# Kernel optimization log

Hardware: AMD Instinct MI355X
Metric: run time of the kernel (lower is better)

## Reference

```python
import jax, jax.numpy as jnp
import numpy as np
import math

JOINT_NAMES = ['pelvis', 'hip_R', 'hip_L', 'knee_R', 'knee_L', 'ankle_R', 'ankle_L', 'trunk', 'shoulder_R', 'shoulder_L', 'elbow_R', 'elbow_L']
KINEMATIC_CHAINS = {'pelvis': ['hip_R', 'hip_L', 'trunk'], 'hip_R': ['pelvis', 'knee_R'], 'hip_L': ['pelvis', 'knee_L'], 'knee_R': ['hip_R', 'ankle_R'], 'knee_L': ['hip_L', 'ankle_L'], 'ankle_R': ['knee_R'], 'ankle_L': ['knee_L'], 'trunk': ['pelvis', 'shoulder_R', 'shoulder_L'], 'shoulder_R': ['trunk', 'elbow_R'], 'shoulder_L': ['trunk', 'elbow_L'], 'elbow_R': ['shoulder_R'], 'elbow_L': ['shoulder_L']}

D_MODEL = 128
N_HEADS = 4
HEAD_DIM = D_MODEL // N_HEADS
B = 16384
N = 12

def build_adjacency_matrix():
    n = len(JOINT_NAMES)
    adj = np.zeros((n, n), dtype=np.float32)
    idx = {name: i for i, name in enumerate(JOINT_NAMES)}
    for joint, neighbors in KINEMATIC_CHAINS.items():
        i = idx[joint]
        for nb in neighbors:
            j = idx[nb]
            adj[i, j] = 1.0
            adj[j, i] = 1.0
    adj = adj + np.eye(n, dtype=np.float32)
    return jnp.asarray(adj)

def setup_inputs() -> dict:
    key = jax.random.key(0)
    ks = jax.random.split(key, 12)
    s = 1.0 / math.sqrt(D_MODEL)  # torch Linear default init scale
    inp = {
        'x': jax.random.normal(ks[0], (B, N, D_MODEL), dtype=jnp.float32),
        'visibility': jax.random.uniform(ks[1], (B, N), dtype=jnp.float32),
        'Wq': jax.random.uniform(ks[2], (D_MODEL, D_MODEL), jnp.float32, -s, s),
        'bq': jax.random.uniform(ks[3], (D_MODEL,), jnp.float32, -s, s),
        'Wk': jax.random.uniform(ks[4], (D_MODEL, D_MODEL), jnp.float32, -s, s),
        'bk': jax.random.uniform(ks[5], (D_MODEL,), jnp.float32, -s, s),
        'Wv': jax.random.uniform(ks[6], (D_MODEL, D_MODEL), jnp.float32, -s, s),
        'bv': jax.random.uniform(ks[7], (D_MODEL,), jnp.float32, -s, s),
        'Wo': jax.random.uniform(ks[8], (D_MODEL, D_MODEL), jnp.float32, -s, s),
        'bo': jax.random.uniform(ks[9], (D_MODEL,), jnp.float32, -s, s),
        'bias_scale': jnp.asarray(1.0, dtype=jnp.float32),
        'adjacency': build_adjacency_matrix(),
    }
    return inp

def reference(x, visibility, Wq, bq, Wk, bk, Wv, bv, Wo, bo, bias_scale, adjacency):
    Bsz, Nj, D = x.shape
    # projections; weights stored as (out,in) like torch Linear -> x @ W.T + b
    def proj(W, b):
        return (jnp.einsum('bnd,ed->bne', x, W) + b).reshape(Bsz, Nj, N_HEADS, HEAD_DIM).transpose(0, 2, 1, 3)
    q = proj(Wq, bq)  # (B, H, N, hd)
    k = proj(Wk, bk)
    v = proj(Wv, bv)
    scores = jnp.einsum('bhnd,bhmd->bhnm', q, k) / math.sqrt(HEAD_DIM)
    scores = scores + adjacency[None, None, :, :] * bias_scale
    # visibility mask: subtract 10 where key joint is not visible
    scores = scores - 10.0 * (1.0 - visibility[:, None, None, :])
    attn = jax.nn.softmax(scores, axis=-1)
    out = jnp.einsum('bhnm,bhmd->bhnd', attn, v)
    out = out.transpose(0, 2, 1, 3).reshape(Bsz, Nj, D)
    out = jnp.einsum('bnd,ed->bne', out, Wo) + bo
    return out
```

## Files before the change

kernel.cpp:

```cpp
#include <hip/hip_runtime.h>


typedef unsigned short u16;
typedef short bf16x8 __attribute__((ext_vector_type(8)));
typedef short bf16x4 __attribute__((ext_vector_type(4)));
typedef float f32x4 __attribute__((ext_vector_type(4)));

#define MFMA(a, b, c) __builtin_amdgcn_mfma_f32_16x16x32_bf16((a), (b), (c), 0, 0, 0)

#define BPW   4
#define ROWS  (BPW * 12)
#define XPAD  136
#define VPAD  20
#define PPAD  20

struct SMem {
    u16   qs[ROWS * XPAD];
    u16   ks[ROWS * XPAD];
    u16   vT[BPW * 128 * VPAD];
    u16   P[4 * 16 * PPAD];
    float bias_s[16 * 16];
    float vis_s[BPW * 16];
    float bvec[4 * 128];
    float rls[4 * 16];
};

__device__ __forceinline__ u16 f2b(float f) {
    unsigned u = __builtin_bit_cast(unsigned, f);
    return (u16)((u + 0x7fffu + ((u >> 16) & 1u)) >> 16);
}

__device__ __forceinline__ void st4(u16* p, float a, float b, float c, float d) {
    ushort4 v; v.x = f2b(a); v.y = f2b(b); v.z = f2b(c); v.w = f2b(d);
    *(ushort4*)p = v;
}

__device__ __forceinline__ bf16x8 pack8(float4 a, float4 b) {
    bf16x8 r;
    r[0] = (short)f2b(a.x); r[1] = (short)f2b(a.y);
    r[2] = (short)f2b(a.z); r[3] = (short)f2b(a.w);
    r[4] = (short)f2b(b.x); r[5] = (short)f2b(b.y);
    r[6] = (short)f2b(b.z); r[7] = (short)f2b(b.w);
    return r;
}

__global__ void prep_w(const float* __restrict__ Wq, const float* __restrict__ Wk,
                       const float* __restrict__ Wv, const float* __restrict__ Wo,
                       u16* __restrict__ wbf) {
    int i = blockIdx.x * 256 + threadIdx.x;
    wbf[i]         = f2b(Wq[i]);
    wbf[16384 + i] = f2b(Wk[i]);
    wbf[32768 + i] = f2b(Wv[i]);
    wbf[49152 + i] = f2b(Wo[i]);
}

__global__ __launch_bounds__(256, 3) void cja_main(
    const float* __restrict__ x, const float* __restrict__ vis,
    const float* __restrict__ bq, const float* __restrict__ bk,
    const float* __restrict__ bv, const float* __restrict__ bo,
    const float* __restrict__ bias_scale, const float* __restrict__ adj,
    const u16* __restrict__ wbf, float* __restrict__ out)
{
    extern __shared__ char smraw[];
    SMem& sm = *(SMem*)smraw;

    const int tid  = threadIdx.x;
    const int wave = tid >> 6;
    const int lane = tid & 63;
    const int lq   = lane >> 4;
    const int lm   = lane & 15;
    const int b0   = blockIdx.x * BPW;

    for (int i = tid; i < BPW * 128; i += 256) {
        unsigned* d = (unsigned*)(sm.vT + i * VPAD + 12);
        d[0] = 0u; d[1] = 0u; d[2] = 0u; d[3] = 0u;
    }
    {
        const float L2E = 1.4426950408889634f;
        float scale = bias_scale[0] * L2E;
        int n = tid >> 4, m = tid & 15;
        float bval;
        if (m >= 12)     bval = -1e30f;
        else if (n < 12) bval = adj[n * 12 + m] * scale;
        else             bval = 0.0f;
        sm.bias_s[tid] = bval;
        if (tid < BPW * 16) {
            int bb = tid >> 4, mm = tid & 15;
            sm.vis_s[tid] = (mm < 12) ? 10.0f * L2E * (1.0f - vis[(size_t)(b0 + bb) * 12 + mm])
                                      : 0.0f;
        }
        if (tid < 128) {
            sm.bvec[tid]       = bq[tid];
            sm.bvec[128 + tid] = bk[tid];
            sm.bvec[256 + tid] = bv[tid];
            sm.bvec[384 + tid] = bo[tid];
        }
    }
    __syncthreads();

    {
        const u16* Wq_b = wbf;
        const u16* Wk_b = wbf + 16384;
        const u16* Wv_b = wbf + 32768;
        const float* xw = x + (size_t)b0 * 1536;
        f32x4 accq[2][3], acck[2][3], accv[3][2];
        #pragma unroll
        for (int i = 0; i < 2; i++)
            #pragma unroll
            for (int j = 0; j < 3; j++) { accq[i][j] = (f32x4){0,0,0,0}; acck[i][j] = (f32x4){0,0,0,0}; }
        #pragma unroll
        for (int i = 0; i < 3; i++)
            #pragma unroll
            for (int j = 0; j < 2; j++) accv[i][j] = (f32x4){0,0,0,0};

        const int mrow0 = wave * 32 + lm;
        const int mrow1 = mrow0 + 16;
        #pragma unroll
        for (int ks2 = 0; ks2 < 4; ks2++) {
            const int koff = ks2 * 32 + lq * 8;
            bf16x8 xf[3];
            #pragma unroll
            for (int nt = 0; nt < 3; nt++) {
                const float* xp = xw + (nt * 16 + lm) * 128 + koff;
                float4 u0 = *(const float4*)xp;
                float4 u1 = *(const float4*)(xp + 4);
                xf[nt] = pack8(u0, u1);
            }
            bf16x8 wq0 = *(const bf16x8*)(Wq_b + mrow0 * 128 + koff);
            bf16x8 wq1 = *(const bf16x8*)(Wq_b + mrow1 * 128 + koff);
            bf16x8 wk0 = *(const bf16x8*)(Wk_b + mrow0 * 128 + koff);
            bf16x8 wk1 = *(const bf16x8*)(Wk_b + mrow1 * 128 + koff);
            bf16x8 wv0 = *(const bf16x8*)(Wv_b + mrow0 * 128 + koff);
            bf16x8 wv1 = *(const bf16x8*)(Wv_b + mrow1 * 128 + koff);
            #pragma unroll
            for (int nt = 0; nt < 3; nt++) {
                accq[0][nt] = MFMA(wq0, xf[nt], accq[0][nt]);
                accq[1][nt] = MFMA(wq1, xf[nt], accq[1][nt]);
                acck[0][nt] = MFMA(wk0, xf[nt], acck[0][nt]);
                acck[1][nt] = MFMA(wk1, xf[nt], acck[1][nt]);
                accv[nt][0] = MFMA(xf[nt], wv0, accv[nt][0]);
                accv[nt][1] = MFMA(xf[nt], wv1, accv[nt][1]);
            }
        }
        #pragma unroll
        for (int mi = 0; mi < 2; mi++) {
            const int e0 = (wave * 2 + mi) * 16 + lq * 4;
            float bq0 = sm.bvec[e0], bq1 = sm.bvec[e0+1], bq2 = sm.bvec[e0+2], bq3 = sm.bvec[e0+3];
            float bk0 = sm.bvec[128+e0], bk1 = sm.bvec[128+e0+1], bk2 = sm.bvec[128+e0+2], bk3 = sm.bvec[128+e0+3];
            #pragma unroll
            for (int nt = 0; nt < 3; nt++) {
                const int n = nt * 16 + lm;
                st4(sm.qs + n * XPAD + e0, accq[mi][nt][0]+bq0, accq[mi][nt][1]+bq1,
                                           accq[mi][nt][2]+bq2, accq[mi][nt][3]+bq3);
                st4(sm.ks + n * XPAD + e0, acck[mi][nt][0]+bk0, acck[mi][nt][1]+bk1,
                                           acck[mi][nt][2]+bk2, acck[mi][nt][3]+bk3);
            }
        }
        #pragma unroll
        for (int nt2 = 0; nt2 < 2; nt2++) {
            const int e = (wave * 2 + nt2) * 16 + lm;
            const float bvv = sm.bvec[256 + e];
            #pragma unroll
            for (int mt = 0; mt < 3; mt++) {
                #pragma unroll
                for (int r = 0; r < 4; r++) {
                    int n = mt * 16 + lq * 4 + r;
                    int bb = n / 12, j = n - bb * 12;
                    sm.vT[bb * (128 * VPAD) + e * VPAD + j] = f2b(accv[mt][nt2][r] + bvv);
                }
            }
        }
    }
    __syncthreads();

    {
        const int bl   = wave;
        const int nql  = (lm < 12) ? lm : 11;
        const u16* qrowp = sm.qs + (bl * 12 + nql) * XPAD;
        const u16* krowp = sm.ks + (bl * 12 + nql) * XPAD;
        const float vism = sm.vis_s[bl * 16 + lm];
        float bias_b[4];
        #pragma unroll
        for (int r = 0; r < 4; r++) bias_b[r] = sm.bias_s[(lq * 4 + r) * 16 + lm];
        u16*   Pw  = sm.P + wave * (16 * PPAD);
        float* rlw = sm.rls + wave * 16;
        const u16* vTb = sm.vT + bl * (128 * VPAD);
        const float SC2 = 0.2550348606381560f;
        const bf16x8 z8 = {0,0,0,0,0,0,0,0};
        #pragma unroll
        for (int h = 0; h < 4; h++) {
            bf16x8 qa = *(const bf16x8*)(qrowp + h * 32 + lq * 8);
            bf16x8 kb = *(const bf16x8*)(krowp + h * 32 + lq * 8);
            f32x4 sc = MFMA(qa, kb, ((f32x4){0,0,0,0}));
            #pragma unroll
            for (int r = 0; r < 4; r++) {
                float s2 = sc[r] * SC2 + bias_b[r] - vism;
                float e  = __builtin_amdgcn_exp2f(s2);
                float l  = e;
                l += __shfl_xor(l, 1, 16);
                l += __shfl_xor(l, 2, 16);
                l += __shfl_xor(l, 4, 16);
                l += __shfl_xor(l, 8, 16);
                Pw[(lq * 4 + r) * PPAD + lm] = f2b(e);
                if (lm == 0) rlw[lq * 4 + r] = __builtin_amdgcn_rcpf(l);
            }
            float rln = rlw[lm];
            bf16x8 pb = z8;
            if (lq < 2) {
                const bf16x4* pp = (const bf16x4*)(Pw + lm * PPAD + lq * 8);
                pb = __builtin_shufflevector(pp[0], pp[1], 0, 1, 2, 3, 4, 5, 6, 7);
            }
            #pragma unroll
            for (int mt = 0; mt < 2; mt++) {
                bf16x8 va = z8;
                if (lq < 2) {
                    const bf16x4* vp = (const bf16x4*)(vTb + (h * 32 + mt * 16 + lm) * VPAD + lq * 8);
                    va = __builtin_shufflevector(vp[0], vp[1], 0, 1, 2, 3, 4, 5, 6, 7);
                }
                f32x4 c = MFMA(va, pb, ((f32x4){0,0,0,0}));
                if (lm < 12) {
                    u16* d = sm.qs + (bl * 12 + lm) * XPAD + h * 32 + mt * 16 + lq * 4;
                    st4(d, c[0] * rln, c[1] * rln, c[2] * rln, c[3] * rln);
                }
            }
        }
    }
    __syncthreads();

    {
        const u16* Wo_b = wbf + 49152;
        f32x4 acc[2][3];
        #pragma unroll
        for (int i = 0; i < 2; i++)
            #pragma unroll
            for (int j = 0; j < 3; j++) acc[i][j] = (f32x4){0,0,0,0};
        const int m0 = wave * 32 + lm;
        #pragma unroll
        for (int ks2 = 0; ks2 < 4; ks2++) {
            const int koff = ks2 * 32 + lq * 8;
            bf16x8 a0 = *(const bf16x8*)(Wo_b + m0 * 128 + koff);
            bf16x8 a1 = *(const bf16x8*)(Wo_b + (m0 + 16) * 128 + koff);
            #pragma unroll
            for (int nt = 0; nt < 3; nt++) {
                bf16x8 bfr = *(const bf16x8*)(sm.qs + (nt * 16 + lm) * XPAD + koff);
                acc[0][nt] = MFMA(a0, bfr, acc[0][nt]);
                acc[1][nt] = MFMA(a1, bfr, acc[1][nt]);
            }
        }
        #pragma unroll
        for (int mi = 0; mi < 2; mi++) {
            const int e0 = (wave * 2 + mi) * 16 + lq * 4;
            float bo0 = sm.bvec[384+e0], bo1 = sm.bvec[384+e0+1],
                  bo2 = sm.bvec[384+e0+2], bo3 = sm.bvec[384+e0+3];
            #pragma unroll
            for (int nt = 0; nt < 3; nt++) {
                const int n = nt * 16 + lm;
                float4 o;
                o.x = acc[mi][nt][0] + bo0;
                o.y = acc[mi][nt][1] + bo1;
                o.z = acc[mi][nt][2] + bo2;
                o.w = acc[mi][nt][3] + bo3;
                *(float4*)(out + ((size_t)(b0 * 12 + n) << 7) + e0) = o;
            }
        }
    }
}

extern "C" void kernel_launch(void* const* d_in, const int* in_sizes, int n_in,
                              void* d_out, int out_size, void* d_ws, size_t ws_size,
                              hipStream_t stream) {
    const float* x   = (const float*)d_in[0];
    const float* vis = (const float*)d_in[1];
    const float* Wq  = (const float*)d_in[2];
    const float* bq  = (const float*)d_in[3];
    const float* Wk  = (const float*)d_in[4];
    const float* bk  = (const float*)d_in[5];
    const float* Wv  = (const float*)d_in[6];
    const float* bv  = (const float*)d_in[7];
    const float* Wo  = (const float*)d_in[8];
    const float* bo  = (const float*)d_in[9];
    const float* bs  = (const float*)d_in[10];
    const float* adj = (const float*)d_in[11];
    u16* wbf = (u16*)d_ws;

    prep_w<<<64, 256, 0, stream>>>(Wq, Wk, Wv, Wo, wbf);
    cja_main<<<16384 / BPW, 256, sizeof(SMem), stream>>>(
        x, vis, bq, bk, bv, bo, bs, adj, wbf, (float*)d_out);
}
```

Baseline: 288.2 us.

## Make blocks persistent over four batch groups and prefetch next x during attention

```diff
diff --git a/kernel.cpp b/kernel.cpp
--- a/kernel.cpp
+++ b/kernel.cpp
@@ -13,6 +13,7 @@
 #define XPAD  136
 #define VPAD  20
 #define PPAD  20
+#define GPW   4
 
 struct SMem {
     u16   qs[ROWS * XPAD];
@@ -69,14 +70,35 @@
     const int lane = tid & 63;
     const int lq   = lane >> 4;
     const int lm   = lane & 15;
-    const int b0   = blockIdx.x * BPW;
+    const int grp0 = blockIdx.x * GPW;
+
+    float4 xr[12][2];
+    bf16x8 xf[12];
+
+    auto issue_x = [&](int grp) {
+        const float* xw = x + (size_t)grp * (BPW * 12 * 128);
+        #pragma unroll
+        for (int ks2 = 0; ks2 < 4; ks2++)
+            #pragma unroll
+            for (int nt = 0; nt < 3; nt++) {
+                const float* xp = xw + (nt * 16 + lm) * 128 + ks2 * 32 + lq * 8;
+                xr[ks2 * 3 + nt][0] = *(const float4*)xp;
+                xr[ks2 * 3 + nt][1] = *(const float4*)(xp + 4);
+            }
+    };
+    auto pack_x = [&]() {
+        #pragma unroll
+        for (int i = 0; i < 12; i++) xf[i] = pack8(xr[i][0], xr[i][1]);
+    };
+
+    issue_x(grp0);
 
     for (int i = tid; i < BPW * 128; i += 256) {
         unsigned* d = (unsigned*)(sm.vT + i * VPAD + 12);
         d[0] = 0u; d[1] = 0u; d[2] = 0u; d[3] = 0u;
     }
+    const float L2E = 1.4426950408889634f;
     {
-        const float L2E = 1.4426950408889634f;
         float scale = bias_scale[0] * L2E;
         int n = tid >> 4, m = tid & 15;
         float bval;
@@ -84,11 +106,6 @@
         else if (n < 12) bval = adj[n * 12 + m] * scale;
         else             bval = 0.0f;
         sm.bias_s[tid] = bval;
-        if (tid < BPW * 16) {
-            int bb = tid >> 4, mm = tid & 15;
-            sm.vis_s[tid] = (mm < 12) ? 10.0f * L2E * (1.0f - vis[(size_t)(b0 + bb) * 12 + mm])
-                                      : 0.0f;
-        }
         if (tid < 128) {
             sm.bvec[tid]       = bq[tid];
             sm.bvec[128 + tid] = bk[tid];
@@ -96,171 +113,212 @@
             sm.bvec[384 + tid] = bo[tid];
         }
     }
+    pack_x();
     __syncthreads();
 
+    const int bl  = wave;
+    const int nql = (lm < 12) ? lm : 11;
+    const u16* qrowp = sm.qs + (bl * 12 + nql) * XPAD;
+    const u16* krowp = sm.ks + (bl * 12 + nql) * XPAD;
+    u16*   Pw  = sm.P + wave * (16 * PPAD);
+    float* rlw = sm.rls + wave * 16;
+    const u16* vTb = sm.vT + bl * (128 * VPAD);
+    const int mrow0 = wave * 32 + lm;
+    const int mrow1 = mrow0 + 16;
+    float bias_b[4];
+    #pragma unroll
+    for (int rr = 0; rr < 4; rr++) bias_b[rr] = sm.bias_s[(lq * 4 + rr) * 16 + lm];
+
+    f32x4 oacc[2][3];
+
+    #pragma unroll 1
+    for (int rnd = 0; rnd < GPW; ++rnd) {
+        const int grp = grp0 + rnd;
+        const int b0  = grp * BPW;
+
+        if (rnd > 0) {
+            const int b0p = b0 - BPW;
+            #pragma unroll
+            for (int mi = 0; mi < 2; mi++) {
+                const int e0 = (wave * 2 + mi) * 16 + lq * 4;
+                #pragma unroll
+                for (int nt = 0; nt < 3; nt++) {
+                    const int n = nt * 16 + lm;
+                    *(f32x4*)(out + ((size_t)(b0p * 12 + n) << 7) + e0) = oacc[mi][nt];
+                }
+            }
+        }
+
+        if (tid < 64) {
+            int bb = tid >> 4, mm = tid & 15;
+            sm.vis_s[tid] = (mm < 12) ? 10.0f * L2E * (1.0f - vis[(size_t)(b0 + bb) * 12 + mm])
+                                      : 0.0f;
+        }
+
+        {
+            const u16* Wq_b = wbf;
+            const u16* Wk_b = wbf + 16384;
+            f32x4 accq[2][3], acck[2][3];
+            #pragma unroll
+            for (int i = 0; i < 2; i++)
+                #pragma unroll
+                for (int j = 0; j < 3; j++) { accq[i][j] = (f32x4){0,0,0,0}; acck[i][j] = (f32x4){0,0,0,0}; }
+            #pragma unroll
+            for (int ks2 = 0; ks2 < 4; ks2++) {
+                const int koff = ks2 * 32 + lq * 8;
+                bf16x8 wq0 = *(const bf16x8*)(Wq_b + mrow0 * 128 + koff);
+                bf16x8 wq1 = *(const bf16x8*)(Wq_b + mrow1 * 128 + koff);
+                bf16x8 wk0 = *(const bf16x8*)(Wk_b + mrow0 * 128 + koff);
+                bf16x8 wk1 = *(const bf16x8*)(Wk_b + mrow1 * 128 + koff);
+                #pragma unroll
+                for (int nt = 0; nt < 3; nt++) {
+                    accq[0][nt] = MFMA(wq0, xf[ks2*3+nt], accq[0][nt]);
+                    accq[1][nt] = MFMA(wq1, xf[ks2*3+nt], accq[1][nt]);
+                    acck[0][nt] = MFMA(wk0, xf[ks2*3+nt], acck[0][nt]);
+                    acck[1][nt] = MFMA(wk1, xf[ks2*3+nt], acck[1][nt]);
+                }
+            }
+            #pragma unroll
+            for (int mi = 0; mi < 2; mi++) {
+                const int e0 = (wave * 2 + mi) * 16 + lq * 4;
+                float bq0 = sm.bvec[e0], bq1 = sm.bvec[e0+1], bq2 = sm.bvec[e0+2], bq3 = sm.bvec[e0+3];
+                float bk0 = sm.bvec[128+e0], bk1 = sm.bvec[128+e0+1], bk2 = sm.bvec[128+e0+2], bk3 = sm.bvec[128+e0+3];
+                #pragma unroll
+                for (int nt = 0; nt < 3; nt++) {
+                    const int n = nt * 16 + lm;
+                    st4(sm.qs + n * XPAD + e0, accq[mi][nt][0]+bq0, accq[mi][nt][1]+bq1,
+                                               accq[mi][nt][2]+bq2, accq[mi][nt][3]+bq3);
+                    st4(sm.ks + n * XPAD + e0, acck[mi][nt][0]+bk0, acck[mi][nt][1]+bk1,
+                                               acck[mi][nt][2]+bk2, acck[mi][nt][3]+bk3);
+                }
+            }
+            const u16* Wv_b = wbf + 32768;
+            f32x4 accv[3][2];
+            #pragma unroll
+            for (int i = 0; i < 3; i++)
+                #pragma unroll
+                for (int j = 0; j < 2; j++) accv[i][j] = (f32x4){0,0,0,0};
+            #pragma unroll
+            for (int ks2 = 0; ks2 < 4; ks2++) {
+                const int koff = ks2 * 32 + lq * 8;
+                bf16x8 wv0 = *(const bf16x8*)(Wv_b + mrow0 * 128 + koff);
+                bf16x8 wv1 = *(const bf16x8*)(Wv_b + mrow1 * 128 + koff);
+                #pragma unroll
+                for (int nt = 0; nt < 3; nt++) {
+                    accv[nt][0] = MFMA(xf[ks2*3+nt], wv0, accv[nt][0]);
+                    accv[nt][1] = MFMA(xf[ks2*3+nt], wv1, accv[nt][1]);
+                }
+            }
+            #pragma unroll
+            for (int nt2 = 0; nt2 < 2; nt2++) {
+                const int e = (wave * 2 + nt2) * 16 + lm;
+                const float bvv = sm.bvec[256 + e];
+                #pragma unroll
+                for (int mt = 0; mt < 3; mt++) {
+                    #pragma unroll
+                    for (int r = 0; r < 4; r++) {
+                        int n = mt * 16 + lq * 4 + r;
+                        int bb = n / 12, j = n - bb * 12;
+                        sm.vT[bb * (128 * VPAD) + e * VPAD + j] = f2b(accv[mt][nt2][r] + bvv);
+                    }
+                }
+            }
+        }
+        __syncthreads();
+
+        {
+            if (rnd + 1 < GPW) issue_x(grp + 1);
+
+            const float vism = sm.vis_s[bl * 16 + lm];
+            const float SC2 = 0.2550348606381560f;
+            const bf16x8 z8 = {0,0,0,0,0,0,0,0};
+            #pragma unroll
+            for (int h = 0; h < 4; h++) {
+                bf16x8 qa = *(const bf16x8*)(qrowp + h * 32 + lq * 8);
+                bf16x8 kb = *(const bf16x8*)(krowp + h * 32 + lq * 8);
+                f32x4 sc = MFMA(qa, kb, ((f32x4){0,0,0,0}));
+                #pragma unroll
+                for (int r = 0; r < 4; r++) {
+                    float s2 = sc[r] * SC2 + bias_b[r] - vism;
+                    float e  = __builtin_amdgcn_exp2f(s2);
+                    float l  = e;
+                    l += __shfl_xor(l, 1, 16);
+                    l += __shfl_xor(l, 2, 16);
+                    l += __shfl_xor(l, 4, 16);
+                    l += __shfl_xor(l, 8, 16);
+                    Pw[(lq * 4 + r) * PPAD + lm] = f2b(e);
+                    if (lm == 0) rlw[lq * 4 + r] = __builtin_amdgcn_rcpf(l);
+                }
+                float rln = rlw[lm];
+                bf16x8 pb = z8;
+                if (lq < 2) {
+                    const bf16x4* pp = (const bf16x4*)(Pw + lm * PPAD + lq * 8);
+                    pb = __builtin_shufflevector(pp[0], pp[1], 0, 1, 2, 3, 4, 5, 6, 7);
+                }
+                #pragma unroll
+                for (int mt = 0; mt < 2; mt++) {
+                    bf16x8 va = z8;
+                    if (lq < 2) {
+                        const bf16x4* vp = (const bf16x4*)(vTb + (h * 32 + mt * 16 + lm) * VPAD + lq * 8);
+                        va = __builtin_shufflevector(vp[0], vp[1], 0, 1, 2, 3, 4, 5, 6, 7);
+                    }
+                    f32x4 c = MFMA(va, pb, ((f32x4){0,0,0,0}));
+                    if (lm < 12) {
+                        u16* d = sm.qs + (bl * 12 + lm) * XPAD + h * 32 + mt * 16 + lq * 4;
+                        st4(d, c[0] * rln, c[1] * rln, c[2] * rln, c[3] * rln);
+                    }
+                }
+            }
+
+            if (rnd + 1 < GPW) pack_x();
+        }
+        __syncthreads();
+
+        {
+            const u16* Wo_b = wbf + 49152;
+            f32x4 acc[2][3];
+            #pragma unroll
+            for (int i = 0; i < 2; i++)
+                #pragma unroll
+                for (int j = 0; j < 3; j++) acc[i][j] = (f32x4){0,0,0,0};
+            #pragma unroll
+            for (int ks2 = 0; ks2 < 4; ks2++) {
+                const int koff = ks2 * 32 + lq * 8;
+                bf16x8 a0 = *(const bf16x8*)(Wo_b + mrow0 * 128 + koff);
+                bf16x8 a1 = *(const bf16x8*)(Wo_b + (mrow1) * 128 + koff);
+                #pragma unroll
+                for (int nt = 0; nt < 3; nt++) {
+                    bf16x8 bfr = *(const bf16x8*)(sm.qs + (nt * 16 + lm) * XPAD + koff);
+                    acc[0][nt] = MFMA(a0, bfr, acc[0][nt]);
+                    acc[1][nt] = MFMA(a1, bfr, acc[1][nt]);
+                }
+            }
+            #pragma unroll
+            for (int mi = 0; mi < 2; mi++) {
+                const int e0 = (wave * 2 + mi) * 16 + lq * 4;
+                float bo0 = sm.bvec[384+e0], bo1 = sm.bvec[384+e0+1],
+                      bo2 = sm.bvec[384+e0+2], bo3 = sm.bvec[384+e0+3];
+                #pragma unroll
+                for (int nt = 0; nt < 3; nt++) {
+                    oacc[mi][nt][0] = acc[mi][nt][0] + bo0;
+                    oacc[mi][nt][1] = acc[mi][nt][1] + bo1;
+                    oacc[mi][nt][2] = acc[mi][nt][2] + bo2;
+                    oacc[mi][nt][3] = acc[mi][nt][3] + bo3;
+                }
+            }
+        }
+        if (rnd + 1 < GPW) __syncthreads();
+    }
+
     {
-        const u16* Wq_b = wbf;
-        const u16* Wk_b = wbf + 16384;
-        const u16* Wv_b = wbf + 32768;
-        const float* xw = x + (size_t)b0 * 1536;
-        f32x4 accq[2][3], acck[2][3], accv[3][2];
-        #pragma unroll
-        for (int i = 0; i < 2; i++)
-            #pragma unroll
-            for (int j = 0; j < 3; j++) { accq[i][j] = (f32x4){0,0,0,0}; acck[i][j] = (f32x4){0,0,0,0}; }
-        #pragma unroll
-        for (int i = 0; i < 3; i++)
-            #pragma unroll
-            for (int j = 0; j < 2; j++) accv[i][j] = (f32x4){0,0,0,0};
-
-        const int mrow0 = wave * 32 + lm;
-        const int mrow1 = mrow0 + 16;
-        #pragma unroll
-        for (int ks2 = 0; ks2 < 4; ks2++) {
-            const int koff = ks2 * 32 + lq * 8;
-            bf16x8 xf[3];
-            #pragma unroll
-            for (int nt = 0; nt < 3; nt++) {
-                const float* xp = xw + (nt * 16 + lm) * 128 + koff;
-                float4 u0 = *(const float4*)xp;
-                float4 u1 = *(const float4*)(xp + 4);
-                xf[nt] = pack8(u0, u1);
-            }
-            bf16x8 wq0 = *(const bf16x8*)(Wq_b + mrow0 * 128 + koff);
-            bf16x8 wq1 = *(const bf16x8*)(Wq_b + mrow1 * 128 + koff);
-            bf16x8 wk0 = *(const bf16x8*)(Wk_b + mrow0 * 128 + koff);
-            bf16x8 wk1 = *(const bf16x8*)(Wk_b + mrow1 * 128 + koff);
-            bf16x8 wv0 = *(const bf16x8*)(Wv_b + mrow0 * 128 + koff);
-            bf16x8 wv1 = *(const bf16x8*)(Wv_b + mrow1 * 128 + koff);
-            #pragma unroll
-            for (int nt = 0; nt < 3; nt++) {
-                accq[0][nt] = MFMA(wq0, xf[nt], accq[0][nt]);
-                accq[1][nt] = MFMA(wq1, xf[nt], accq[1][nt]);
-                acck[0][nt] = MFMA(wk0, xf[nt], acck[0][nt]);
-                acck[1][nt] = MFMA(wk1, xf[nt], acck[1][nt]);
-                accv[nt][0] = MFMA(xf[nt], wv0, accv[nt][0]);
-                accv[nt][1] = MFMA(xf[nt], wv1, accv[nt][1]);
-            }
-        }
+        const int b0p = (grp0 + GPW - 1) * BPW;
         #pragma unroll
         for (int mi = 0; mi < 2; mi++) {
             const int e0 = (wave * 2 + mi) * 16 + lq * 4;
-            float bq0 = sm.bvec[e0], bq1 = sm.bvec[e0+1], bq2 = sm.bvec[e0+2], bq3 = sm.bvec[e0+3];
-            float bk0 = sm.bvec[128+e0], bk1 = sm.bvec[128+e0+1], bk2 = sm.bvec[128+e0+2], bk3 = sm.bvec[128+e0+3];
             #pragma unroll
             for (int nt = 0; nt < 3; nt++) {
                 const int n = nt * 16 + lm;
-                st4(sm.qs + n * XPAD + e0, accq[mi][nt][0]+bq0, accq[mi][nt][1]+bq1,
-                                           accq[mi][nt][2]+bq2, accq[mi][nt][3]+bq3);
-                st4(sm.ks + n * XPAD + e0, acck[mi][nt][0]+bk0, acck[mi][nt][1]+bk1,
-                                           acck[mi][nt][2]+bk2, acck[mi][nt][3]+bk3);
-            }
-        }
-        #pragma unroll
-        for (int nt2 = 0; nt2 < 2; nt2++) {
-            const int e = (wave * 2 + nt2) * 16 + lm;
-            const float bvv = sm.bvec[256 + e];
-            #pragma unroll
-            for (int mt = 0; mt < 3; mt++) {
-                #pragma unroll
-                for (int r = 0; r < 4; r++) {
-                    int n = mt * 16 + lq * 4 + r;
-                    int bb = n / 12, j = n - bb * 12;
-                    sm.vT[bb * (128 * VPAD) + e * VPAD + j] = f2b(accv[mt][nt2][r] + bvv);
-                }
-            }
-        }
-    }
-    __syncthreads();
-
-    {
-        const int bl   = wave;
-        const int nql  = (lm < 12) ? lm : 11;
-        const u16* qrowp = sm.qs + (bl * 12 + nql) * XPAD;
-        const u16* krowp = sm.ks + (bl * 12 + nql) * XPAD;
-        const float vism = sm.vis_s[bl * 16 + lm];
-        float bias_b[4];
-        #pragma unroll
-        for (int r = 0; r < 4; r++) bias_b[r] = sm.bias_s[(lq * 4 + r) * 16 + lm];
-        u16*   Pw  = sm.P + wave * (16 * PPAD);
-        float* rlw = sm.rls + wave * 16;
-        const u16* vTb = sm.vT + bl * (128 * VPAD);
-        const float SC2 = 0.2550348606381560f;
-        const bf16x8 z8 = {0,0,0,0,0,0,0,0};
-        #pragma unroll
-        for (int h = 0; h < 4; h++) {
-            bf16x8 qa = *(const bf16x8*)(qrowp + h * 32 + lq * 8);
-            bf16x8 kb = *(const bf16x8*)(krowp + h * 32 + lq * 8);
-            f32x4 sc = MFMA(qa, kb, ((f32x4){0,0,0,0}));
-            #pragma unroll
-            for (int r = 0; r < 4; r++) {
-                float s2 = sc[r] * SC2 + bias_b[r] - vism;
-                float e  = __builtin_amdgcn_exp2f(s2);
-                float l  = e;
-                l += __shfl_xor(l, 1, 16);
-                l += __shfl_xor(l, 2, 16);
-                l += __shfl_xor(l, 4, 16);
-                l += __shfl_xor(l, 8, 16);
-                Pw[(lq * 4 + r) * PPAD + lm] = f2b(e);
-                if (lm == 0) rlw[lq * 4 + r] = __builtin_amdgcn_rcpf(l);
-            }
-            float rln = rlw[lm];
-            bf16x8 pb = z8;
-            if (lq < 2) {
-                const bf16x4* pp = (const bf16x4*)(Pw + lm * PPAD + lq * 8);
-                pb = __builtin_shufflevector(pp[0], pp[1], 0, 1, 2, 3, 4, 5, 6, 7);
-            }
-            #pragma unroll
-            for (int mt = 0; mt < 2; mt++) {
-                bf16x8 va = z8;
-                if (lq < 2) {
-                    const bf16x4* vp = (const bf16x4*)(vTb + (h * 32 + mt * 16 + lm) * VPAD + lq * 8);
-                    va = __builtin_shufflevector(vp[0], vp[1], 0, 1, 2, 3, 4, 5, 6, 7);
-                }
-                f32x4 c = MFMA(va, pb, ((f32x4){0,0,0,0}));
-                if (lm < 12) {
-                    u16* d = sm.qs + (bl * 12 + lm) * XPAD + h * 32 + mt * 16 + lq * 4;
-                    st4(d, c[0] * rln, c[1] * rln, c[2] * rln, c[3] * rln);
-                }
-            }
-        }
-    }
-    __syncthreads();
-
-    {
-        const u16* Wo_b = wbf + 49152;
-        f32x4 acc[2][3];
-        #pragma unroll
-        for (int i = 0; i < 2; i++)
-            #pragma unroll
-            for (int j = 0; j < 3; j++) acc[i][j] = (f32x4){0,0,0,0};
-        const int m0 = wave * 32 + lm;
-        #pragma unroll
-        for (int ks2 = 0; ks2 < 4; ks2++) {
-            const int koff = ks2 * 32 + lq * 8;
-            bf16x8 a0 = *(const bf16x8*)(Wo_b + m0 * 128 + koff);
-            bf16x8 a1 = *(const bf16x8*)(Wo_b + (m0 + 16) * 128 + koff);
-            #pragma unroll
-            for (int nt = 0; nt < 3; nt++) {
-                bf16x8 bfr = *(const bf16x8*)(sm.qs + (nt * 16 + lm) * XPAD + koff);
-                acc[0][nt] = MFMA(a0, bfr, acc[0][nt]);
-                acc[1][nt] = MFMA(a1, bfr, acc[1][nt]);
-            }
-        }
-        #pragma unroll
-        for (int mi = 0; mi < 2; mi++) {
-            const int e0 = (wave * 2 + mi) * 16 + lq * 4;
-            float bo0 = sm.bvec[384+e0], bo1 = sm.bvec[384+e0+1],
-                  bo2 = sm.bvec[384+e0+2], bo3 = sm.bvec[384+e0+3];
-            #pragma unroll
-            for (int nt = 0; nt < 3; nt++) {
-                const int n = nt * 16 + lm;
-                float4 o;
-                o.x = acc[mi][nt][0] + bo0;
-                o.y = acc[mi][nt][1] + bo1;
-                o.z = acc[mi][nt][2] + bo2;
-                o.w = acc[mi][nt][3] + bo3;
-                *(float4*)(out + ((size_t)(b0 * 12 + n) << 7) + e0) = o;
+                *(f32x4*)(out + ((size_t)(b0p * 12 + n) << 7) + e0) = oacc[mi][nt];
             }
         }
     }
@@ -284,6 +342,6 @@
     u16* wbf = (u16*)d_ws;
 
     prep_w<<<64, 256, 0, stream>>>(Wq, Wk, Wv, Wo, wbf);
-    cja_main<<<16384 / BPW, 256, sizeof(SMem), stream>>>(
+    cja_main<<<16384 / (BPW * GPW), 256, sizeof(SMem), stream>>>(
         x, vis, bq, bk, bv, bo, bs, adj, wbf, (float*)d_out);
 }
```

After: 533.7 us. 1.85x slower.

## Make main kernel persistent and compute softmax via transposed scores with shuffles

Applied to the files above, without the earlier changes.

```diff
diff --git a/kernel.cpp b/kernel.cpp
--- a/kernel.cpp
+++ b/kernel.cpp
@@ -5,6 +5,7 @@
 typedef short bf16x8 __attribute__((ext_vector_type(8)));
 typedef short bf16x4 __attribute__((ext_vector_type(4)));
 typedef float f32x4 __attribute__((ext_vector_type(4)));
+typedef unsigned int u32x4 __attribute__((ext_vector_type(4)));
 
 #define MFMA(a, b, c) __builtin_amdgcn_mfma_f32_16x16x32_bf16((a), (b), (c), 0, 0, 0)
 
@@ -12,17 +13,15 @@
 #define ROWS  (BPW * 12)
 #define XPAD  136
 #define VPAD  20
-#define PPAD  20
+#define NGRP  4096
+#define GRID  768
 
 struct SMem {
     u16   qs[ROWS * XPAD];
     u16   ks[ROWS * XPAD];
     u16   vT[BPW * 128 * VPAD];
-    u16   P[4 * 16 * PPAD];
     float bias_s[16 * 16];
-    float vis_s[BPW * 16];
     float bvec[4 * 128];
-    float rls[4 * 16];
 };
 
 __device__ __forceinline__ u16 f2b(float f) {
@@ -69,14 +68,13 @@
     const int lane = tid & 63;
     const int lq   = lane >> 4;
     const int lm   = lane & 15;
-    const int b0   = blockIdx.x * BPW;
 
     for (int i = tid; i < BPW * 128; i += 256) {
         unsigned* d = (unsigned*)(sm.vT + i * VPAD + 12);
         d[0] = 0u; d[1] = 0u; d[2] = 0u; d[3] = 0u;
     }
+    const float L2E = 1.4426950408889634f;
     {
-        const float L2E = 1.4426950408889634f;
         float scale = bias_scale[0] * L2E;
         int n = tid >> 4, m = tid & 15;
         float bval;
@@ -84,11 +82,6 @@
         else if (n < 12) bval = adj[n * 12 + m] * scale;
         else             bval = 0.0f;
         sm.bias_s[tid] = bval;
-        if (tid < BPW * 16) {
-            int bb = tid >> 4, mm = tid & 15;
-            sm.vis_s[tid] = (mm < 12) ? 10.0f * L2E * (1.0f - vis[(size_t)(b0 + bb) * 12 + mm])
-                                      : 0.0f;
-        }
         if (tid < 128) {
             sm.bvec[tid]       = bq[tid];
             sm.bvec[128 + tid] = bk[tid];
@@ -98,171 +91,183 @@
     }
     __syncthreads();
 
-    {
-        const u16* Wq_b = wbf;
-        const u16* Wk_b = wbf + 16384;
-        const u16* Wv_b = wbf + 32768;
-        const float* xw = x + (size_t)b0 * 1536;
-        f32x4 accq[2][3], acck[2][3], accv[3][2];
-        #pragma unroll
-        for (int i = 0; i < 2; i++)
-            #pragma unroll
-            for (int j = 0; j < 3; j++) { accq[i][j] = (f32x4){0,0,0,0}; acck[i][j] = (f32x4){0,0,0,0}; }
-        #pragma unroll
-        for (int i = 0; i < 3; i++)
-            #pragma unroll
-            for (int j = 0; j < 2; j++) accv[i][j] = (f32x4){0,0,0,0};
-
-        const int mrow0 = wave * 32 + lm;
-        const int mrow1 = mrow0 + 16;
-        #pragma unroll
-        for (int ks2 = 0; ks2 < 4; ks2++) {
-            const int koff = ks2 * 32 + lq * 8;
-            bf16x8 xf[3];
-            #pragma unroll
-            for (int nt = 0; nt < 3; nt++) {
-                const float* xp = xw + (nt * 16 + lm) * 128 + koff;
-                float4 u0 = *(const float4*)xp;
-                float4 u1 = *(const float4*)(xp + 4);
-                xf[nt] = pack8(u0, u1);
-            }
-            bf16x8 wq0 = *(const bf16x8*)(Wq_b + mrow0 * 128 + koff);
-            bf16x8 wq1 = *(const bf16x8*)(Wq_b + mrow1 * 128 + koff);
-            bf16x8 wk0 = *(const bf16x8*)(Wk_b + mrow0 * 128 + koff);
-            bf16x8 wk1 = *(const bf16x8*)(Wk_b + mrow1 * 128 + koff);
-            bf16x8 wv0 = *(const bf16x8*)(Wv_b + mrow0 * 128 + koff);
-            bf16x8 wv1 = *(const bf16x8*)(Wv_b + mrow1 * 128 + koff);
-            #pragma unroll
-            for (int nt = 0; nt < 3; nt++) {
-                accq[0][nt] = MFMA(wq0, xf[nt], accq[0][nt]);
-                accq[1][nt] = MFMA(wq1, xf[nt], accq[1][nt]);
-                acck[0][nt] = MFMA(wk0, xf[nt], acck[0][nt]);
-                acck[1][nt] = MFMA(wk1, xf[nt], acck[1][nt]);
-                accv[nt][0] = MFMA(xf[nt], wv0, accv[nt][0]);
-                accv[nt][1] = MFMA(xf[nt], wv1, accv[nt][1]);
-            }
-        }
-        #pragma unroll
-        for (int mi = 0; mi < 2; mi++) {
-            const int e0 = (wave * 2 + mi) * 16 + lq * 4;
-            float bq0 = sm.bvec[e0], bq1 = sm.bvec[e0+1], bq2 = sm.bvec[e0+2], bq3 = sm.bvec[e0+3];
-            float bk0 = sm.bvec[128+e0], bk1 = sm.bvec[128+e0+1], bk2 = sm.bvec[128+e0+2], bk3 = sm.bvec[128+e0+3];
-            #pragma unroll
-            for (int nt = 0; nt < 3; nt++) {
-                const int n = nt * 16 + lm;
-                st4(sm.qs + n * XPAD + e0, accq[mi][nt][0]+bq0, accq[mi][nt][1]+bq1,
-                                           accq[mi][nt][2]+bq2, accq[mi][nt][3]+bq3);
-                st4(sm.ks + n * XPAD + e0, acck[mi][nt][0]+bk0, acck[mi][nt][1]+bk1,
-                                           acck[mi][nt][2]+bk2, acck[mi][nt][3]+bk3);
-            }
-        }
-        #pragma unroll
-        for (int nt2 = 0; nt2 < 2; nt2++) {
-            const int e = (wave * 2 + nt2) * 16 + lm;
-            const float bvv = sm.bvec[256 + e];
-            #pragma unroll
-            for (int mt = 0; mt < 3; mt++) {
-                #pragma unroll
-                for (int r = 0; r < 4; r++) {
-                    int n = mt * 16 + lq * 4 + r;
-                    int bb = n / 12, j = n - bb * 12;
-                    sm.vT[bb * (128 * VPAD) + e * VPAD + j] = f2b(accv[mt][nt2][r] + bvv);
-                }
-            }
-        }
-    }
-    __syncthreads();
-
-    {
-        const int bl   = wave;
-        const int nql  = (lm < 12) ? lm : 11;
-        const u16* qrowp = sm.qs + (bl * 12 + nql) * XPAD;
-        const u16* krowp = sm.ks + (bl * 12 + nql) * XPAD;
-        const float vism = sm.vis_s[bl * 16 + lm];
-        float bias_b[4];
-        #pragma unroll
-        for (int r = 0; r < 4; r++) bias_b[r] = sm.bias_s[(lq * 4 + r) * 16 + lm];
-        u16*   Pw  = sm.P + wave * (16 * PPAD);
-        float* rlw = sm.rls + wave * 16;
-        const u16* vTb = sm.vT + bl * (128 * VPAD);
-        const float SC2 = 0.2550348606381560f;
-        const bf16x8 z8 = {0,0,0,0,0,0,0,0};
-        #pragma unroll
-        for (int h = 0; h < 4; h++) {
-            bf16x8 qa = *(const bf16x8*)(qrowp + h * 32 + lq * 8);
-            bf16x8 kb = *(const bf16x8*)(krowp + h * 32 + lq * 8);
-            f32x4 sc = MFMA(qa, kb, ((f32x4){0,0,0,0}));
-            #pragma unroll
-            for (int r = 0; r < 4; r++) {
-                float s2 = sc[r] * SC2 + bias_b[r] - vism;
-                float e  = __builtin_amdgcn_exp2f(s2);
-                float l  = e;
-                l += __shfl_xor(l, 1, 16);
-                l += __shfl_xor(l, 2, 16);
-                l += __shfl_xor(l, 4, 16);
-                l += __shfl_xor(l, 8, 16);
-                Pw[(lq * 4 + r) * PPAD + lm] = f2b(e);
-                if (lm == 0) rlw[lq * 4 + r] = __builtin_amdgcn_rcpf(l);
-            }
-            float rln = rlw[lm];
-            bf16x8 pb = z8;
-            if (lq < 2) {
-                const bf16x4* pp = (const bf16x4*)(Pw + lm * PPAD + lq * 8);
-                pb = __builtin_shufflevector(pp[0], pp[1], 0, 1, 2, 3, 4, 5, 6, 7);
-            }
-            #pragma unroll
-            for (int mt = 0; mt < 2; mt++) {
-                bf16x8 va = z8;
-                if (lq < 2) {
-                    const bf16x4* vp = (const bf16x4*)(vTb + (h * 32 + mt * 16 + lm) * VPAD + lq * 8);
-                    va = __builtin_shufflevector(vp[0], vp[1], 0, 1, 2, 3, 4, 5, 6, 7);
-                }
-                f32x4 c = MFMA(va, pb, ((f32x4){0,0,0,0}));
-                if (lm < 12) {
-                    u16* d = sm.qs + (bl * 12 + lm) * XPAD + h * 32 + mt * 16 + lq * 4;
-                    st4(d, c[0] * rln, c[1] * rln, c[2] * rln, c[3] * rln);
-                }
-            }
-        }
-    }
-    __syncthreads();
-
-    {
-        const u16* Wo_b = wbf + 49152;
-        f32x4 acc[2][3];
-        #pragma unroll
-        for (int i = 0; i < 2; i++)
-            #pragma unroll
-            for (int j = 0; j < 3; j++) acc[i][j] = (f32x4){0,0,0,0};
-        const int m0 = wave * 32 + lm;
-        #pragma unroll
-        for (int ks2 = 0; ks2 < 4; ks2++) {
-            const int koff = ks2 * 32 + lq * 8;
-            bf16x8 a0 = *(const bf16x8*)(Wo_b + m0 * 128 + koff);
-            bf16x8 a1 = *(const bf16x8*)(Wo_b + (m0 + 16) * 128 + koff);
-            #pragma unroll
-            for (int nt = 0; nt < 3; nt++) {
-                bf16x8 bfr = *(const bf16x8*)(sm.qs + (nt * 16 + lm) * XPAD + koff);
-                acc[0][nt] = MFMA(a0, bfr, acc[0][nt]);
-                acc[1][nt] = MFMA(a1, bfr, acc[1][nt]);
-            }
-        }
-        #pragma unroll
-        for (int mi = 0; mi < 2; mi++) {
-            const int e0 = (wave * 2 + mi) * 16 + lq * 4;
-            float bo0 = sm.bvec[384+e0], bo1 = sm.bvec[384+e0+1],
-                  bo2 = sm.bvec[384+e0+2], bo3 = sm.bvec[384+e0+3];
-            #pragma unroll
-            for (int nt = 0; nt < 3; nt++) {
-                const int n = nt * 16 + lm;
-                float4 o;
-                o.x = acc[mi][nt][0] + bo0;
-                o.y = acc[mi][nt][1] + bo1;
-                o.z = acc[mi][nt][2] + bo2;
-                o.w = acc[mi][nt][3] + bo3;
-                *(float4*)(out + ((size_t)(b0 * 12 + n) << 7) + e0) = o;
-            }
-        }
+    const int bl  = wave;
+    const int nql = (lm < 12) ? lm : 11;
+    const u16* qrowp = sm.qs + (bl * 12 + nql) * XPAD;
+    const u16* krowp = sm.ks + (bl * 12 + nql) * XPAD;
+    const u16* vTb = sm.vT + bl * (128 * VPAD);
+    const int mrow0 = wave * 32 + lm;
+    const int mrow1 = mrow0 + 16;
+    float biasv[4];
+    #pragma unroll
+    for (int rr = 0; rr < 4; rr++) biasv[rr] = sm.bias_s[lm * 16 + lq * 4 + rr];
+    const int s0 = ((lq << 1) << 4) + lm;
+    const int s1 = s0 + 16;
+    const float vc = (lq < 3) ? 10.0f * L2E : 0.0f;
+
+    #pragma unroll 1
+    for (int grp = blockIdx.x; grp < NGRP; grp += GRID) {
+        const int  b0      = grp * BPW;
+        const bool hasNext = (grp + GRID) < NGRP;
+
+        const float* vp = vis + (size_t)(b0 + bl) * 12 + (lq < 3 ? lq * 4 : 0);
+        float4 vv = *(const float4*)vp;
+
+        {
+            const u16* Wq_b = wbf;
+            const u16* Wk_b = wbf + 16384;
+            const u16* Wv_b = wbf + 32768;
+            const float* xw = x + (size_t)b0 * 1536;
+            f32x4 accq[2][3], acck[2][3], accv[3][2];
+            #pragma unroll
+            for (int i = 0; i < 2; i++)
+                #pragma unroll
+                for (int j = 0; j < 3; j++) { accq[i][j] = (f32x4){0,0,0,0}; acck[i][j] = (f32x4){0,0,0,0}; }
+            #pragma unroll
+            for (int i = 0; i < 3; i++)
+                #pragma unroll
+                for (int j = 0; j < 2; j++) accv[i][j] = (f32x4){0,0,0,0};
+            #pragma unroll
+            for (int ks2 = 0; ks2 < 4; ks2++) {
+                const int koff = ks2 * 32 + lq * 8;
+                bf16x8 xt[3];
+                #pragma unroll
+                for (int nt = 0; nt < 3; nt++) {
+                    const float* xp = xw + (nt * 16 + lm) * 128 + koff;
+                    float4 u0 = *(const float4*)xp;
+                    float4 u1 = *(const float4*)(xp + 4);
+                    xt[nt] = pack8(u0, u1);
+                }
+                bf16x8 wq0 = *(const bf16x8*)(Wq_b + mrow0 * 128 + koff);
+                bf16x8 wq1 = *(const bf16x8*)(Wq_b + mrow1 * 128 + koff);
+                bf16x8 wk0 = *(const bf16x8*)(Wk_b + mrow0 * 128 + koff);
+                bf16x8 wk1 = *(const bf16x8*)(Wk_b + mrow1 * 128 + koff);
+                bf16x8 wv0 = *(const bf16x8*)(Wv_b + mrow0 * 128 + koff);
+                bf16x8 wv1 = *(const bf16x8*)(Wv_b + mrow1 * 128 + koff);
+                #pragma unroll
+                for (int nt = 0; nt < 3; nt++) {
+                    accq[0][nt] = MFMA(wq0, xt[nt], accq[0][nt]);
+                    accq[1][nt] = MFMA(wq1, xt[nt], accq[1][nt]);
+                    acck[0][nt] = MFMA(wk0, xt[nt], acck[0][nt]);
+                    acck[1][nt] = MFMA(wk1, xt[nt], acck[1][nt]);
+                    accv[nt][0] = MFMA(xt[nt], wv0, accv[nt][0]);
+                    accv[nt][1] = MFMA(xt[nt], wv1, accv[nt][1]);
+                }
+            }
+            #pragma unroll
+            for (int mi = 0; mi < 2; mi++) {
+                const int e0 = (wave * 2 + mi) * 16 + lq * 4;
+                float bq0 = sm.bvec[e0], bq1 = sm.bvec[e0+1], bq2 = sm.bvec[e0+2], bq3 = sm.bvec[e0+3];
+                float bk0 = sm.bvec[128+e0], bk1 = sm.bvec[128+e0+1], bk2 = sm.bvec[128+e0+2], bk3 = sm.bvec[128+e0+3];
+                #pragma unroll
+                for (int nt = 0; nt < 3; nt++) {
+                    const int n = nt * 16 + lm;
+                    st4(sm.qs + n * XPAD + e0, accq[mi][nt][0]+bq0, accq[mi][nt][1]+bq1,
+                                               accq[mi][nt][2]+bq2, accq[mi][nt][3]+bq3);
+                    st4(sm.ks + n * XPAD + e0, acck[mi][nt][0]+bk0, acck[mi][nt][1]+bk1,
+                                               acck[mi][nt][2]+bk2, acck[mi][nt][3]+bk3);
+                }
+            }
+            #pragma unroll
+            for (int nt2 = 0; nt2 < 2; nt2++) {
+                const int e = (wave * 2 + nt2) * 16 + lm;
+                const float bvv = sm.bvec[256 + e];
+                #pragma unroll
+                for (int mt = 0; mt < 3; mt++) {
+                    #pragma unroll
+                    for (int r = 0; r < 4; r++) {
+                        int n = mt * 16 + lq * 4 + r;
+                        int bb = n / 12, j = n - bb * 12;
+                        sm.vT[bb * (128 * VPAD) + e * VPAD + j] = f2b(accv[mt][nt2][r] + bvv);
+                    }
+                }
+            }
+        }
+        __syncthreads();
+
+        {
+            const float SC2 = 0.2550348606381560f;
+            const bf16x8 z8 = {0,0,0,0,0,0,0,0};
+            float visr[4];
+            visr[0] = vc * (1.0f - vv.x); visr[1] = vc * (1.0f - vv.y);
+            visr[2] = vc * (1.0f - vv.z); visr[3] = vc * (1.0f - vv.w);
+            #pragma unroll
+            for (int h = 0; h < 4; h++) {
+                bf16x8 qa = *(const bf16x8*)(qrowp + h * 32 + lq * 8);
+                bf16x8 kb = *(const bf16x8*)(krowp + h * 32 + lq * 8);
+                f32x4 sc = MFMA(kb, qa, ((f32x4){0,0,0,0}));
+                float e0 = __builtin_amdgcn_exp2f(sc[0] * SC2 + biasv[0] - visr[0]);
+                float e1 = __builtin_amdgcn_exp2f(sc[1] * SC2 + biasv[1] - visr[1]);
+                float e2 = __builtin_amdgcn_exp2f(sc[2] * SC2 + biasv[2] - visr[2]);
+                float e3 = __builtin_amdgcn_exp2f(sc[3] * SC2 + biasv[3] - visr[3]);
+                float l = (e0 + e1) + (e2 + e3);
+                l += __shfl_xor(l, 16);
+                l += __shfl_xor(l, 32);
+                float rln = __builtin_amdgcn_rcpf(l);
+                unsigned w0 = (unsigned)f2b(e0) | ((unsigned)f2b(e1) << 16);
+                unsigned w1 = (unsigned)f2b(e2) | ((unsigned)f2b(e3) << 16);
+                unsigned p0 = (unsigned)__shfl((int)w0, s0);
+                unsigned p1 = (unsigned)__shfl((int)w1, s0);
+                unsigned p2 = (unsigned)__shfl((int)w0, s1);
+                unsigned p3 = (unsigned)__shfl((int)w1, s1);
+                u32x4 pw;
+                pw[0] = (lq < 2) ? p0 : 0u;  pw[1] = (lq < 2) ? p1 : 0u;
+                pw[2] = (lq < 2) ? p2 : 0u;  pw[3] = (lq < 2) ? p3 : 0u;
+                bf16x8 pb = __builtin_bit_cast(bf16x8, pw);
+                #pragma unroll
+                for (int mt = 0; mt < 2; mt++) {
+                    bf16x8 va = z8;
+                    if (lq < 2) {
+                        const bf16x4* vp2 = (const bf16x4*)(vTb + (h * 32 + mt * 16 + lm) * VPAD + lq * 8);
+                        va = __builtin_shufflevector(vp2[0], vp2[1], 0, 1, 2, 3, 4, 5, 6, 7);
+                    }
+                    f32x4 c = MFMA(va, pb, ((f32x4){0,0,0,0}));
+                    if (lm < 12) {
+                        u16* d = sm.qs + (bl * 12 + lm) * XPAD + h * 32 + mt * 16 + lq * 4;
+                        st4(d, c[0] * rln, c[1] * rln, c[2] * rln, c[3] * rln);
+                    }
+                }
+            }
+        }
+        __syncthreads();
+
+        {
+            const u16* Wo_b = wbf + 49152;
+            f32x4 acc[2][3];
+            #pragma unroll
+            for (int i = 0; i < 2; i++)
+                #pragma unroll
+                for (int j = 0; j < 3; j++) acc[i][j] = (f32x4){0,0,0,0};
+            #pragma unroll
+            for (int ks2 = 0; ks2 < 4; ks2++) {
+                const int koff = ks2 * 32 + lq * 8;
+                bf16x8 a0 = *(const bf16x8*)(Wo_b + mrow0 * 128 + koff);
+                bf16x8 a1 = *(const bf16x8*)(Wo_b + mrow1 * 128 + koff);
+                #pragma unroll
+                for (int nt = 0; nt < 3; nt++) {
+                    bf16x8 bfr = *(const bf16x8*)(sm.qs + (nt * 16 + lm) * XPAD + koff);
+                    acc[0][nt] = MFMA(a0, bfr, acc[0][nt]);
+                    acc[1][nt] = MFMA(a1, bfr, acc[1][nt]);
+                }
+            }
+            #pragma unroll
+            for (int mi = 0; mi < 2; mi++) {
+                const int e0 = (wave * 2 + mi) * 16 + lq * 4;
+                float bo0 = sm.bvec[384+e0], bo1 = sm.bvec[384+e0+1],
+                      bo2 = sm.bvec[384+e0+2], bo3 = sm.bvec[384+e0+3];
+                #pragma unroll
+                for (int nt = 0; nt < 3; nt++) {
+                    const int n = nt * 16 + lm;
+                    float4 o;
+                    o.x = acc[mi][nt][0] + bo0;
+                    o.y = acc[mi][nt][1] + bo1;
+                    o.z = acc[mi][nt][2] + bo2;
+                    o.w = acc[mi][nt][3] + bo3;
+                    *(float4*)(out + ((size_t)(b0 * 12 + n) << 7) + e0) = o;
+                }
+            }
+        }
+        if (hasNext) __syncthreads();
     }
 }
 
@@ -284,6 +289,6 @@
     u16* wbf = (u16*)d_ws;
 
     prep_w<<<64, 256, 0, stream>>>(Wq, Wk, Wv, Wo, wbf);
-    cja_main<<<16384 / BPW, 256, sizeof(SMem), stream>>>(
+    cja_main<<<GRID, 256, sizeof(SMem), stream>>>(
         x, vis, bq, bk, bv, bo, bs, adj, wbf, (float*)d_out);
 }
```

After: 358.0 us. +24.2%, slower.
